# Kernel optimization log

Hardware: AMD Instinct MI355X
Metric: run time of the kernel (lower is better)

## Reference

```python
import jax, jax.numpy as jnp
import numpy as np

N_NODES = 100000
N_EDGES = 1600000
D_IN = 64
D_OUT = 64


def setup_inputs() -> dict:
    key = jax.random.key(0)
    k1, k2, k3, k4, k5, k6, k7 = jax.random.split(key, 7)
    x = jax.random.normal(k1, (N_NODES, D_IN), dtype=jnp.float32)
    edge_index = jax.random.randint(k2, (2, N_EDGES), 0, N_NODES, dtype=jnp.int64)
    pos_encoding = jax.random.normal(k3, (N_NODES, D_IN), dtype=jnp.float32)
    # GCNConv linear weight (no bias inside lin; bias added post-aggregation)
    W_gcn = jax.random.normal(k4, (D_IN, D_OUT), dtype=jnp.float32) / np.sqrt(D_IN)
    b_gcn = jax.random.normal(k5, (D_OUT,), dtype=jnp.float32) * 0.01
    # positional encoding Linear
    W_pos = jax.random.normal(k6, (D_IN, D_OUT), dtype=jnp.float32) / np.sqrt(D_IN)
    b_pos = jax.random.normal(k7, (D_OUT,), dtype=jnp.float32) * 0.01
    return {"x": x, "edge_index": edge_index, "pos_encoding": pos_encoding,
            "W_gcn": W_gcn, "b_gcn": b_gcn, "W_pos": W_pos, "b_pos": b_pos}


def _gcn_conv(x, edge_index, W, b):
    n = x.shape[0]
    # add self-loops (PyG GCNConv default)
    loop = jnp.arange(n, dtype=edge_index.dtype)
    src = jnp.concatenate([edge_index[0], loop])
    dst = jnp.concatenate([edge_index[1], loop])
    # symmetric normalization: deg over destination with unit edge weights
    deg = jax.ops.segment_sum(jnp.ones_like(src, dtype=x.dtype), dst, num_segments=n)
    dinv = jnp.where(deg > 0, jax.lax.rsqrt(deg), 0.0)
    norm = dinv[src] * dinv[dst]  # [E+N]
    h = x @ W  # [N, D_OUT]
    msg = h[src] * norm[:, None]  # gather + scale
    out = jax.ops.segment_sum(msg, dst, num_segments=n)  # scatter-add
    return out + b


def reference(x, edge_index, pos_encoding, W_gcn, b_gcn, W_pos, b_pos):
    conv_out = _gcn_conv(x, edge_index, W_gcn, b_gcn)
    pos = pos_encoding @ W_pos + b_pos
    return conv_out + pos
```

## Files before the change

kernel.cpp:

```cpp
#include <hip/hip_runtime.h>
#include <hip/hip_fp16.h>

#define NN 100000
#define NE 1600000
#define D  64

#define B1    1024
#define BSH   9
#define BMSK  511
#define NB    196
#define M     (NB * B1)

typedef __attribute__((ext_vector_type(8))) _Float16 f16x8;
typedef __attribute__((ext_vector_type(4))) float    f32x4;

__global__ __launch_bounds__(256) void k_hist(const int* __restrict__ dst,
                                              int* __restrict__ hist) {
    __shared__ int h[NB];
    int t = threadIdx.x, blk = blockIdx.x;
    for (int i = t; i < NB; i += 256) h[i] = 0;
    __syncthreads();
    for (int e = blk * 256 + t; e < NE; e += B1 * 256)
        atomicAdd(&h[dst[e] >> BSH], 1);
    __syncthreads();
    for (int i = t; i < NB; i += 256) hist[i * B1 + blk] = h[i];
}

__global__ __launch_bounds__(1024) void k_scanA(int* __restrict__ hist,
                                                int* __restrict__ binsum) {
    __shared__ int ps[1024];
    int t = threadIdx.x, b = blockIdx.x;
    int v = hist[b * B1 + t];
    ps[t] = v;
    __syncthreads();
    for (int off = 1; off < 1024; off <<= 1) {
        int u = (t >= off) ? ps[t - off] : 0;
        __syncthreads();
        ps[t] += u;
        __syncthreads();
    }
    hist[b * B1 + t] = ps[t] - v;
    if (t == 1023) binsum[b] = ps[t];
}

__global__ __launch_bounds__(256) void k_scanB(const int* __restrict__ binsum,
                                               int* __restrict__ binoff) {
    __shared__ int ps[256];
    int t = threadIdx.x;
    int v = (t < NB) ? binsum[t] : 0;
    ps[t] = v;
    __syncthreads();
    for (int off = 1; off < 256; off <<= 1) {
        int u = (t >= off) ? ps[t - off] : 0;
        __syncthreads();
        ps[t] += u;
        __syncthreads();
    }
    if (t < NB) binoff[t] = ps[t] - v;
    if (t == NB - 1) binoff[NB] = ps[t];
}

__global__ __launch_bounds__(256) void k_scatter1(
    const int* __restrict__ src, const int* __restrict__ dst,
    const int* __restrict__ hist, const int* __restrict__ binoff,
    unsigned* __restrict__ ebuf)
{
    __shared__ int cur[NB];
    int t = threadIdx.x, blk = blockIdx.x;
    for (int i = t; i < NB; i += 256)
        cur[i] = binoff[i] + hist[i * B1 + blk];
    __syncthreads();
    for (int e = blk * 256 + t; e < NE; e += B1 * 256) {
        int d = dst[e];
        int p = atomicAdd(&cur[d >> BSH], 1);
        ebuf[p] = ((unsigned)src[e] << BSH) | (unsigned)(d & BMSK);
    }
}

__global__ __launch_bounds__(512) void k_build(
    const int* __restrict__ binoff, const unsigned* __restrict__ ebuf,
    int* __restrict__ rs, float* __restrict__ dinv, int* __restrict__ bucket)
{
    __shared__ int c[512];
    __shared__ int ps[512];
    int t = threadIdx.x, b = blockIdx.x;
    int e0 = binoff[b], e1 = binoff[b + 1];
    c[t] = 0;
    __syncthreads();
    for (int e = e0 + t; e < e1; e += 512)
        atomicAdd(&c[ebuf[e] & BMSK], 1);
    __syncthreads();
    int a = c[t];
    ps[t] = a;
    __syncthreads();
    for (int off = 1; off < 512; off <<= 1) {
        int u = (t >= off) ? ps[t - off] : 0;
        __syncthreads();
        ps[t] += u;
        __syncthreads();
    }
    int p = e0 + ps[t] - a;
    int node = (b << BSH) + t;
    if (node < NN) { rs[node] = p; dinv[node] = rsqrtf((float)(a + 1)); }
    if (b == NB - 1 && t == 0) rs[NN] = NE;
    __syncthreads();
    c[t] = p;
    __syncthreads();
    for (int e = e0 + t; e < e1; e += 512) {
        unsigned u = ebuf[e];
        int pp = atomicAdd(&c[u & BMSK], 1);
        bucket[pp] = (int)(u >> BSH);
    }
}

__global__ __launch_bounds__(256) void k_mm(
    const float* __restrict__ x, const float* __restrict__ Wg,
    const float* __restrict__ dinv, __half* __restrict__ g,
    const float* __restrict__ pos, const float* __restrict__ Wp,
    const float* __restrict__ bg, const float* __restrict__ bp,
    float* __restrict__ out)
{
    __shared__ __align__(16) _Float16 Wt[64][64];
    int t = threadIdx.x;
    int lane = t & 63;
    int wid = t >> 6;
    int half_grid = gridDim.x >> 1;
    bool job2 = blockIdx.x >= half_grid;
    int blk = job2 ? (blockIdx.x - half_grid) : blockIdx.x;
    const float* A = job2 ? pos : x;
    const float* W = job2 ? Wp : Wg;

    for (int i = t; i < 64 * 64; i += 256) {
        int k = i >> 6, n = i & 63;
        Wt[n][k] = (_Float16)W[i];
    }
    __syncthreads();

    int lr = lane & 15;
    int lg = lane >> 4;
    int kofs = lg * 8;

    f16x8 b[4][2];
#pragma unroll
    for (int n = 0; n < 4; ++n)
#pragma unroll
        for (int kt = 0; kt < 2; ++kt)
            b[n][kt] = *(const f16x8*)&Wt[n * 16 + lr][kt * 32 + kofs];

    float bsum[4] = {0.f, 0.f, 0.f, 0.f};
    if (job2) {
#pragma unroll
        for (int n = 0; n < 4; ++n) {
            int c = n * 16 + lr;
            bsum[n] = bg[c] + bp[c];
        }
    }

    for (int rb0 = blk * 64; rb0 < NN; rb0 += half_grid * 64) {
        int rb = rb0 + wid * 16;
        int arow = rb + lr;
        int arc = arow < NN ? arow : NN - 1;
        const float4* ap = (const float4*)(A + (long)arc * 64 + kofs);
        float4 p0 = ap[0], p1 = ap[1], p2 = ap[8], p3 = ap[9];
        f16x8 a0, a1;
        a0[0] = (_Float16)p0.x; a0[1] = (_Float16)p0.y;
        a0[2] = (_Float16)p0.z; a0[3] = (_Float16)p0.w;
        a0[4] = (_Float16)p1.x; a0[5] = (_Float16)p1.y;
        a0[6] = (_Float16)p1.z; a0[7] = (_Float16)p1.w;
        a1[0] = (_Float16)p2.x; a1[1] = (_Float16)p2.y;
        a1[2] = (_Float16)p2.z; a1[3] = (_Float16)p2.w;
        a1[4] = (_Float16)p3.x; a1[5] = (_Float16)p3.y;
        a1[6] = (_Float16)p3.z; a1[7] = (_Float16)p3.w;

        f32x4 z = {0.f, 0.f, 0.f, 0.f};
        f32x4 acc[4] = {z, z, z, z};
#pragma unroll
        for (int n = 0; n < 4; ++n) {
            acc[n] = __builtin_amdgcn_mfma_f32_16x16x32_f16(a0, b[n][0], acc[n], 0, 0, 0);
            acc[n] = __builtin_amdgcn_mfma_f32_16x16x32_f16(a1, b[n][1], acc[n], 0, 0, 0);
        }

        int orow0 = rb + lg * 4;
        if (!job2) {
#pragma unroll
            for (int r = 0; r < 4; ++r) {
                int row = orow0 + r;
                if (row < NN) {
                    float di = dinv[row];
#pragma unroll
                    for (int n = 0; n < 4; ++n)
                        g[(long)row * D + n * 16 + lr] = __float2half(acc[n][r] * di);
                }
            }
        } else {
#pragma unroll
            for (int r = 0; r < 4; ++r) {
                int row = orow0 + r;
                if (row < NN) {
#pragma unroll
                    for (int n = 0; n < 4; ++n)
                        out[(long)row * D + n * 16 + lr] = acc[n][r] + bsum[n];
                }
            }
        }
    }
}

__global__ __launch_bounds__(256) void k_gather(
    const int* __restrict__ rs, const int* __restrict__ bucket,
    const float* __restrict__ dinv, const __half* __restrict__ g,
    float* __restrict__ out)
{
    int lane = threadIdx.x & 63;
    int f = lane & 7;
    int grp = lane >> 3;
    int w0 = (blockIdx.x << 2) + (threadIdx.x >> 6);
    int nw = gridDim.x << 2;
    const uint4* gq = (const uint4*)g;

    for (int n0 = w0; n0 < NN; n0 += nw) {
        int node = __builtin_amdgcn_readfirstlane(n0);
        int r0 = rs[node], r1 = rs[node + 1];
        float a0 = 0.f, a1 = 0.f, a2 = 0.f, a3 = 0.f;
        float a4 = 0.f, a5 = 0.f, a6 = 0.f, a7 = 0.f;
        for (int base = r0; base < r1; base += 64) {
            int nl = r1 - base; if (nl > 64) nl = 64;
            int sl = (lane < nl) ? bucket[base + lane] : 0;
#pragma unroll 2
            for (int c = 0; c < nl; c += 8) {
                int ei = c + grp;
                int s = __shfl(sl, ei);
                if (ei < nl) {
                    uint4 u = gq[(long)s * 8 + f];
                    __half2 h0 = *(__half2*)&u.x, h1 = *(__half2*)&u.y;
                    __half2 h2 = *(__half2*)&u.z, h3 = *(__half2*)&u.w;
                    a0 += __low2float(h0); a1 += __high2float(h0);
                    a2 += __low2float(h1); a3 += __high2float(h1);
                    a4 += __low2float(h2); a5 += __high2float(h2);
                    a6 += __low2float(h3); a7 += __high2float(h3);
                }
            }
        }
#pragma unroll
        for (int mask = 8; mask <= 32; mask <<= 1) {
            a0 += __shfl_xor(a0, mask); a1 += __shfl_xor(a1, mask);
            a2 += __shfl_xor(a2, mask); a3 += __shfl_xor(a3, mask);
            a4 += __shfl_xor(a4, mask); a5 += __shfl_xor(a5, mask);
            a6 += __shfl_xor(a6, mask); a7 += __shfl_xor(a7, mask);
        }
        if (lane < 16) {
            int ff = lane & 7, hs = lane >> 3;
            uint4 u = gq[(long)node * 8 + ff];
            __half2 s0 = hs ? *(__half2*)&u.z : *(__half2*)&u.x;
            __half2 s1 = hs ? *(__half2*)&u.w : *(__half2*)&u.y;
            float b0 = hs ? a4 : a0, b1 = hs ? a5 : a1;
            float b2 = hs ? a6 : a2, b3 = hs ? a7 : a3;
            float di = dinv[node];
            float4* op = (float4*)(out + (long)node * D) + (ff * 2 + hs);
            float4 o = *op;
            o.x += (b0 + __low2float(s0)) * di;
            o.y += (b1 + __high2float(s0)) * di;
            o.z += (b2 + __low2float(s1)) * di;
            o.w += (b3 + __high2float(s1)) * di;
            *op = o;
        }
    }
}

extern "C" void kernel_launch(void* const* d_in, const int* in_sizes, int n_in,
                              void* d_out, int out_size, void* d_ws, size_t ws_size,
                              hipStream_t stream) {
    const float* x   = (const float*)d_in[0];
    const int*   ei  = (const int*)d_in[1];
    const float* pos = (const float*)d_in[2];
    const float* Wg  = (const float*)d_in[3];
    const float* bg  = (const float*)d_in[4];
    const float* Wp  = (const float*)d_in[5];
    const float* bp  = (const float*)d_in[6];
    float* out = (float*)d_out;

    const int* src = ei;
    const int* dst = ei + NE;

    int*      bucket = (int*)d_ws;
    int*      hist   = (int*)d_ws;
    unsigned* ebuf   = (unsigned*)(bucket + NE);
    int*      rs     = (int*)(ebuf + NE);
    float*    dinv   = (float*)(rs + NN + 4);
    __half*   g      = (__half*)(dinv + NN);
    int*      binsum = (int*)(g + (size_t)NN * D);
    int*      binoff = binsum + NB;

    hipLaunchKernelGGL(k_hist,     dim3(B1),   dim3(256),  0, stream, dst, hist);
    hipLaunchKernelGGL(k_scanA,    dim3(NB),   dim3(1024), 0, stream, hist, binsum);
    hipLaunchKernelGGL(k_scanB,    dim3(1),    dim3(256),  0, stream, binsum, binoff);
    hipLaunchKernelGGL(k_scatter1, dim3(B1),   dim3(256),  0, stream, src, dst, hist, binoff, ebuf);
    hipLaunchKernelGGL(k_build,    dim3(NB),   dim3(512),  0, stream, binoff, ebuf, rs, dinv, bucket);
    hipLaunchKernelGGL(k_mm,       dim3(1564), dim3(256),  0, stream,
                       x, Wg, dinv, g, pos, Wp, bg, bp, out);
    hipLaunchKernelGGL(k_gather,   dim3(2048), dim3(256),  0, stream,
                       rs, bucket, dinv, g, out);
}
```

Measured before the change: 215.5 us.

## Fuse histogram and scatter into one pass with per-bin fixed-stride buffers

Replaces the histogram, two-level scan and scatter kernels with one fused kernel. Each block counts its edges per bin in shared memory, reserves a range per bin through global atomics, and writes into fixed-stride per-bin regions. This reads the edge list once instead of twice and removes the large per-block histogram scan. The gather loop drops its per-edge bounds check by padding with a zero row at index NN, and the workspace is aliased so g overlaps ebuf. The fixed bin stride assumes no bin holds more than 16256 edges, which holds for uniform random inputs but could overflow on skewed graphs.

Measured after the change: 217.5 us. No clear change (+0.9%).

```diff
diff --git a/kernel.cpp b/kernel.cpp
--- a/kernel.cpp
+++ b/kernel.cpp
@@ -5,49 +5,56 @@
 #define NE 1600000
 #define D  64
 
-#define B1    1024
-#define BSH   9
-#define BMSK  511
-#define NB    196
-#define M     (NB * B1)
+#define B1     1024
+#define BSH    9
+#define BMSK   511
+#define NB     196
+#define STRIDE 16256
 
 typedef __attribute__((ext_vector_type(8))) _Float16 f16x8;
 typedef __attribute__((ext_vector_type(4))) float    f32x4;
 
-__global__ __launch_bounds__(256) void k_hist(const int* __restrict__ dst,
-                                              int* __restrict__ hist) {
+__global__ __launch_bounds__(256) void k_scatter_fused(
+    const int* __restrict__ src, const int* __restrict__ dst,
+    int* __restrict__ gcnt, unsigned* __restrict__ ebuf)
+{
     __shared__ int h[NB];
     int t = threadIdx.x, blk = blockIdx.x;
     for (int i = t; i < NB; i += 256) h[i] = 0;
     __syncthreads();
-    for (int e = blk * 256 + t; e < NE; e += B1 * 256)
-        atomicAdd(&h[dst[e] >> BSH], 1);
-    __syncthreads();
-    for (int i = t; i < NB; i += 256) hist[i * B1 + blk] = h[i];
-}
-
-__global__ __launch_bounds__(1024) void k_scanA(int* __restrict__ hist,
-                                                int* __restrict__ binsum) {
-    __shared__ int ps[1024];
-    int t = threadIdx.x, b = blockIdx.x;
-    int v = hist[b * B1 + t];
-    ps[t] = v;
-    __syncthreads();
-    for (int off = 1; off < 1024; off <<= 1) {
-        int u = (t >= off) ? ps[t - off] : 0;
-        __syncthreads();
-        ps[t] += u;
-        __syncthreads();
-    }
-    hist[b * B1 + t] = ps[t] - v;
-    if (t == 1023) binsum[b] = ps[t];
-}
-
-__global__ __launch_bounds__(256) void k_scanB(const int* __restrict__ binsum,
-                                               int* __restrict__ binoff) {
+    unsigned v[7]; int bn[7]; int cntl = 0;
+    int e = blk * 256 + t;
+#pragma unroll
+    for (int i = 0; i < 7; ++i, e += B1 * 256) {
+        if (e < NE) {
+            int d = dst[e];
+            int s = src[e];
+            int b = d >> BSH;
+            v[i] = ((unsigned)s << BSH) | (unsigned)(d & BMSK);
+            bn[i] = b;
+            atomicAdd(&h[b], 1);
+            cntl = i + 1;
+        }
+    }
+    __syncthreads();
+    for (int i = t; i < NB; i += 256)
+        h[i] = atomicAdd(&gcnt[i], h[i]);
+    __syncthreads();
+#pragma unroll
+    for (int i = 0; i < 7; ++i) {
+        if (i < cntl) {
+            int b = bn[i];
+            int p = atomicAdd(&h[b], 1);
+            ebuf[b * STRIDE + p] = v[i];
+        }
+    }
+}
+
+__global__ __launch_bounds__(256) void k_scan196(const int* __restrict__ gcnt,
+                                                 int* __restrict__ binoff) {
     __shared__ int ps[256];
     int t = threadIdx.x;
-    int v = (t < NB) ? binsum[t] : 0;
+    int v = (t < NB) ? gcnt[t] : 0;
     ps[t] = v;
     __syncthreads();
     for (int off = 1; off < 256; off <<= 1) {
@@ -60,35 +67,21 @@
     if (t == NB - 1) binoff[NB] = ps[t];
 }
 
-__global__ __launch_bounds__(256) void k_scatter1(
-    const int* __restrict__ src, const int* __restrict__ dst,
-    const int* __restrict__ hist, const int* __restrict__ binoff,
-    unsigned* __restrict__ ebuf)
-{
-    __shared__ int cur[NB];
-    int t = threadIdx.x, blk = blockIdx.x;
-    for (int i = t; i < NB; i += 256)
-        cur[i] = binoff[i] + hist[i * B1 + blk];
-    __syncthreads();
-    for (int e = blk * 256 + t; e < NE; e += B1 * 256) {
-        int d = dst[e];
-        int p = atomicAdd(&cur[d >> BSH], 1);
-        ebuf[p] = ((unsigned)src[e] << BSH) | (unsigned)(d & BMSK);
-    }
-}
-
 __global__ __launch_bounds__(512) void k_build(
-    const int* __restrict__ binoff, const unsigned* __restrict__ ebuf,
+    const int* __restrict__ gcnt, const int* __restrict__ binoff,
+    const unsigned* __restrict__ ebuf,
     int* __restrict__ rs, float* __restrict__ dinv, int* __restrict__ bucket)
 {
     __shared__ int c[512];
     __shared__ int ps[512];
     int t = threadIdx.x, b = blockIdx.x;
-    int e0 = binoff[b], e1 = binoff[b + 1];
+    int e0s = b * STRIDE;
+    int cnt = gcnt[b];
+    int g0  = binoff[b];
     c[t] = 0;
     __syncthreads();
-    for (int e = e0 + t; e < e1; e += 512)
-        atomicAdd(&c[ebuf[e] & BMSK], 1);
+    for (int e = t; e < cnt; e += 512)
+        atomicAdd(&c[ebuf[e0s + e] & BMSK], 1);
     __syncthreads();
     int a = c[t];
     ps[t] = a;
@@ -99,15 +92,15 @@
         ps[t] += u;
         __syncthreads();
     }
-    int p = e0 + ps[t] - a;
+    int p = g0 + ps[t] - a;
     int node = (b << BSH) + t;
     if (node < NN) { rs[node] = p; dinv[node] = rsqrtf((float)(a + 1)); }
     if (b == NB - 1 && t == 0) rs[NN] = NE;
     __syncthreads();
     c[t] = p;
     __syncthreads();
-    for (int e = e0 + t; e < e1; e += 512) {
-        unsigned u = ebuf[e];
+    for (int e = t; e < cnt; e += 512) {
+        unsigned u = ebuf[e0s + e];
         int pp = atomicAdd(&c[u & BMSK], 1);
         bucket[pp] = (int)(u >> BSH);
     }
@@ -130,6 +123,8 @@
     const float* A = job2 ? pos : x;
     const float* W = job2 ? Wp : Wg;
 
+    if (blockIdx.x == 0 && t < 64) g[(long)NN * D + t] = __float2half(0.f);
+
     for (int i = t; i < 64 * 64; i += 256) {
         int k = i >> 6, n = i & 63;
         Wt[n][k] = (_Float16)W[i];
@@ -151,8 +146,8 @@
     if (job2) {
 #pragma unroll
         for (int n = 0; n < 4; ++n) {
-            int c = n * 16 + lr;
-            bsum[n] = bg[c] + bp[c];
+            int cc = n * 16 + lr;
+            bsum[n] = bg[cc] + bp[cc];
         }
     }
 
@@ -224,21 +219,20 @@
         float a0 = 0.f, a1 = 0.f, a2 = 0.f, a3 = 0.f;
         float a4 = 0.f, a5 = 0.f, a6 = 0.f, a7 = 0.f;
         for (int base = r0; base < r1; base += 64) {
-            int nl = r1 - base; if (nl > 64) nl = 64;
-            int sl = (lane < nl) ? bucket[base + lane] : 0;
-#pragma unroll 2
-            for (int c = 0; c < nl; c += 8) {
-                int ei = c + grp;
-                int s = __shfl(sl, ei);
-                if (ei < nl) {
-                    uint4 u = gq[(long)s * 8 + f];
-                    __half2 h0 = *(__half2*)&u.x, h1 = *(__half2*)&u.y;
-                    __half2 h2 = *(__half2*)&u.z, h3 = *(__half2*)&u.w;
-                    a0 += __low2float(h0); a1 += __high2float(h0);
-                    a2 += __low2float(h1); a3 += __high2float(h1);
-                    a4 += __low2float(h2); a5 += __high2float(h2);
-                    a6 += __low2float(h3); a7 += __high2float(h3);
-                }
+            int rem = r1 - base;
+            int nl = rem < 64 ? rem : 64;
+            int sl = (lane < nl) ? bucket[base + lane] : NN;
+            int NG = (nl + 7) >> 3;
+#pragma unroll 4
+            for (int c = 0; c < NG; ++c) {
+                int s = __shfl(sl, c * 8 + grp);
+                uint4 u = gq[(long)s * 8 + f];
+                __half2 h0 = *(__half2*)&u.x, h1 = *(__half2*)&u.y;
+                __half2 h2 = *(__half2*)&u.z, h3 = *(__half2*)&u.w;
+                a0 += __low2float(h0); a1 += __high2float(h0);
+                a2 += __low2float(h1); a3 += __high2float(h1);
+                a4 += __low2float(h2); a5 += __high2float(h2);
+                a6 += __low2float(h3); a7 += __high2float(h3);
             }
         }
 #pragma unroll
@@ -282,22 +276,23 @@
     const int* src = ei;
     const int* dst = ei + NE;
 
-    int*      bucket = (int*)d_ws;
-    int*      hist   = (int*)d_ws;
-    unsigned* ebuf   = (unsigned*)(bucket + NE);
-    int*      rs     = (int*)(ebuf + NE);
+    char* Wb = (char*)d_ws;
+    __half*   g      = (__half*)Wb;
+    unsigned* ebuf   = (unsigned*)Wb;
+    int*      bucket = (int*)(Wb + 12800256);
+    int*      rs     = bucket + NE;
     float*    dinv   = (float*)(rs + NN + 4);
-    __half*   g      = (__half*)(dinv + NN);
-    int*      binsum = (int*)(g + (size_t)NN * D);
-    int*      binoff = binsum + NB;
-
-    hipLaunchKernelGGL(k_hist,     dim3(B1),   dim3(256),  0, stream, dst, hist);
-    hipLaunchKernelGGL(k_scanA,    dim3(NB),   dim3(1024), 0, stream, hist, binsum);
-    hipLaunchKernelGGL(k_scanB,    dim3(1),    dim3(256),  0, stream, binsum, binoff);
-    hipLaunchKernelGGL(k_scatter1, dim3(B1),   dim3(256),  0, stream, src, dst, hist, binoff, ebuf);
-    hipLaunchKernelGGL(k_build,    dim3(NB),   dim3(512),  0, stream, binoff, ebuf, rs, dinv, bucket);
-    hipLaunchKernelGGL(k_mm,       dim3(1564), dim3(256),  0, stream,
+    int*      gcnt   = (int*)(dinv + NN);
+    int*      binoff = gcnt + NB;
+
+    hipMemsetAsync(gcnt, 0, NB * sizeof(int), stream);
+    hipLaunchKernelGGL(k_scatter_fused, dim3(B1),   dim3(256), 0, stream,
+                       src, dst, gcnt, ebuf);
+    hipLaunchKernelGGL(k_scan196,       dim3(1),    dim3(256), 0, stream, gcnt, binoff);
+    hipLaunchKernelGGL(k_build,         dim3(NB),   dim3(512), 0, stream,
+                       gcnt, binoff, ebuf, rs, dinv, bucket);
+    hipLaunchKernelGGL(k_mm,            dim3(1564), dim3(256), 0, stream,
                        x, Wg, dinv, g, pos, Wp, bg, bp, out);
-    hipLaunchKernelGGL(k_gather,   dim3(2048), dim3(256),  0, stream,
+    hipLaunchKernelGGL(k_gather,        dim3(2048), dim3(256), 0, stream,
                        rs, bucket, dinv, g, out);
 }
```

## Replace CSR build and pull gather with bin-local LDS atomic scatter aggregation

Applied to the files above, without the earlier changes.

Drops the per-node CSR construction (second counting sort into bucket and rs). Edges are left coarsely binned by 256-node destination ranges, and each bin is aggregated by one 1024-thread block that accumulates into LDS with float atomics before a final per-node write. The aim is to remove the k_build pass and the per-node irregular loops. In exchange the gather becomes LDS-atomic-bound, runs with only 391 blocks, and sums in a nondeterministic order.

Result: slower. 853.0 us (+295.9%).

```diff
diff --git a/kernel.cpp b/kernel.cpp
--- a/kernel.cpp
+++ b/kernel.cpp
@@ -5,11 +5,10 @@
 #define NE 1600000
 #define D  64
 
-#define B1    1024
-#define BSH   9
-#define BMSK  511
-#define NB    196
-#define M     (NB * B1)
+#define B1   1024
+#define BSH  8
+#define BMSK 255
+#define NB   391
 
 typedef __attribute__((ext_vector_type(8))) _Float16 f16x8;
 typedef __attribute__((ext_vector_type(4))) float    f32x4;
@@ -27,7 +26,7 @@
 }
 
 __global__ __launch_bounds__(1024) void k_scanA(int* __restrict__ hist,
-                                                int* __restrict__ binsum) {
+                                                int* __restrict__ bsum) {
     __shared__ int ps[1024];
     int t = threadIdx.x, b = blockIdx.x;
     int v = hist[b * B1 + t];
@@ -40,17 +39,17 @@
         __syncthreads();
     }
     hist[b * B1 + t] = ps[t] - v;
-    if (t == 1023) binsum[b] = ps[t];
-}
-
-__global__ __launch_bounds__(256) void k_scanB(const int* __restrict__ binsum,
+    if (t == 1023) bsum[b] = ps[t];
+}
+
+__global__ __launch_bounds__(512) void k_scanB(const int* __restrict__ bsum,
                                                int* __restrict__ binoff) {
-    __shared__ int ps[256];
+    __shared__ int ps[512];
     int t = threadIdx.x;
-    int v = (t < NB) ? binsum[t] : 0;
+    int v = (t < NB) ? bsum[t] : 0;
     ps[t] = v;
     __syncthreads();
-    for (int off = 1; off < 256; off <<= 1) {
+    for (int off = 1; off < 512; off <<= 1) {
         int u = (t >= off) ? ps[t - off] : 0;
         __syncthreads();
         ps[t] += u;
@@ -77,39 +76,20 @@
     }
 }
 
-__global__ __launch_bounds__(512) void k_build(
-    const int* __restrict__ binoff, const unsigned* __restrict__ ebuf,
-    int* __restrict__ rs, float* __restrict__ dinv, int* __restrict__ bucket)
-{
-    __shared__ int c[512];
-    __shared__ int ps[512];
+__global__ __launch_bounds__(1024) void k_count(const int* __restrict__ binoff,
+                                                const unsigned* __restrict__ ebuf,
+                                                float* __restrict__ dinv) {
+    __shared__ int c[256];
     int t = threadIdx.x, b = blockIdx.x;
+    if (t < 256) c[t] = 0;
+    __syncthreads();
     int e0 = binoff[b], e1 = binoff[b + 1];
-    c[t] = 0;
-    __syncthreads();
-    for (int e = e0 + t; e < e1; e += 512)
+    for (int e = e0 + t; e < e1; e += 1024)
         atomicAdd(&c[ebuf[e] & BMSK], 1);
     __syncthreads();
-    int a = c[t];
-    ps[t] = a;
-    __syncthreads();
-    for (int off = 1; off < 512; off <<= 1) {
-        int u = (t >= off) ? ps[t - off] : 0;
-        __syncthreads();
-        ps[t] += u;
-        __syncthreads();
-    }
-    int p = e0 + ps[t] - a;
-    int node = (b << BSH) + t;
-    if (node < NN) { rs[node] = p; dinv[node] = rsqrtf((float)(a + 1)); }
-    if (b == NB - 1 && t == 0) rs[NN] = NE;
-    __syncthreads();
-    c[t] = p;
-    __syncthreads();
-    for (int e = e0 + t; e < e1; e += 512) {
-        unsigned u = ebuf[e];
-        int pp = atomicAdd(&c[u & BMSK], 1);
-        bucket[pp] = (int)(u >> BSH);
+    if (t < 256) {
+        int node = (b << BSH) + t;
+        if (node < NN) dinv[node] = rsqrtf((float)(c[t] + 1));
     }
 }
 
@@ -151,8 +131,8 @@
     if (job2) {
 #pragma unroll
         for (int n = 0; n < 4; ++n) {
-            int c = n * 16 + lr;
-            bsum[n] = bg[c] + bp[c];
+            int cc = n * 16 + lr;
+            bsum[n] = bg[cc] + bp[cc];
         }
     }
 
@@ -206,63 +186,51 @@
     }
 }
 
-__global__ __launch_bounds__(256) void k_gather(
-    const int* __restrict__ rs, const int* __restrict__ bucket,
+__global__ __launch_bounds__(1024) void k_gather(
+    const int* __restrict__ binoff, const unsigned* __restrict__ ebuf,
     const float* __restrict__ dinv, const __half* __restrict__ g,
     float* __restrict__ out)
 {
-    int lane = threadIdx.x & 63;
-    int f = lane & 7;
-    int grp = lane >> 3;
-    int w0 = (blockIdx.x << 2) + (threadIdx.x >> 6);
-    int nw = gridDim.x << 2;
-    const uint4* gq = (const uint4*)g;
-
-    for (int n0 = w0; n0 < NN; n0 += nw) {
-        int node = __builtin_amdgcn_readfirstlane(n0);
-        int r0 = rs[node], r1 = rs[node + 1];
-        float a0 = 0.f, a1 = 0.f, a2 = 0.f, a3 = 0.f;
-        float a4 = 0.f, a5 = 0.f, a6 = 0.f, a7 = 0.f;
-        for (int base = r0; base < r1; base += 64) {
-            int nl = r1 - base; if (nl > 64) nl = 64;
-            int sl = (lane < nl) ? bucket[base + lane] : 0;
-#pragma unroll 2
-            for (int c = 0; c < nl; c += 8) {
-                int ei = c + grp;
-                int s = __shfl(sl, ei);
-                if (ei < nl) {
-                    uint4 u = gq[(long)s * 8 + f];
-                    __half2 h0 = *(__half2*)&u.x, h1 = *(__half2*)&u.y;
-                    __half2 h2 = *(__half2*)&u.z, h3 = *(__half2*)&u.w;
-                    a0 += __low2float(h0); a1 += __high2float(h0);
-                    a2 += __low2float(h1); a3 += __high2float(h1);
-                    a4 += __low2float(h2); a5 += __high2float(h2);
-                    a6 += __low2float(h3); a7 += __high2float(h3);
-                }
+    __shared__ float accE[256 * 32];
+    __shared__ float accO[256 * 32];
+    int t = threadIdx.x, b = blockIdx.x;
+    for (int i = t; i < 256 * 32; i += 1024) { accE[i] = 0.f; accO[i] = 0.f; }
+    __syncthreads();
+
+    int e0 = binoff[b], e1 = binoff[b + 1];
+    int lane = t & 63;
+    int hl = lane >> 5;
+    int l  = lane & 31;
+    int w  = t >> 6;
+    const unsigned* gw = (const unsigned*)g;
+
+    for (int base = e0 + w * 8; base < e1; base += 16 * 8) {
+#pragma unroll
+        for (int k = 0; k < 4; ++k) {
+            int e = base + k * 2 + hl;
+            if (e < e1) {
+                unsigned u = ebuf[e];
+                int s  = (int)(u >> BSH);
+                int dl = (int)(u & BMSK);
+                unsigned gd = gw[(long)s * 32 + l];
+                __half2 hh = *(__half2*)&gd;
+                atomicAdd(&accE[dl * 32 + l], __low2float(hh));
+                atomicAdd(&accO[dl * 32 + l], __high2float(hh));
             }
         }
-#pragma unroll
-        for (int mask = 8; mask <= 32; mask <<= 1) {
-            a0 += __shfl_xor(a0, mask); a1 += __shfl_xor(a1, mask);
-            a2 += __shfl_xor(a2, mask); a3 += __shfl_xor(a3, mask);
-            a4 += __shfl_xor(a4, mask); a5 += __shfl_xor(a5, mask);
-            a6 += __shfl_xor(a6, mask); a7 += __shfl_xor(a7, mask);
-        }
-        if (lane < 16) {
-            int ff = lane & 7, hs = lane >> 3;
-            uint4 u = gq[(long)node * 8 + ff];
-            __half2 s0 = hs ? *(__half2*)&u.z : *(__half2*)&u.x;
-            __half2 s1 = hs ? *(__half2*)&u.w : *(__half2*)&u.y;
-            float b0 = hs ? a4 : a0, b1 = hs ? a5 : a1;
-            float b2 = hs ? a6 : a2, b3 = hs ? a7 : a3;
+    }
+    __syncthreads();
+
+    int r = t >> 6;
+    for (int p = 0; p < 16; ++p) {
+        int row = p * 16 + r;
+        int node = (b << BSH) + row;
+        if (node < NN) {
             float di = dinv[node];
-            float4* op = (float4*)(out + (long)node * D) + (ff * 2 + hs);
-            float4 o = *op;
-            o.x += (b0 + __low2float(s0)) * di;
-            o.y += (b1 + __high2float(s0)) * di;
-            o.z += (b2 + __low2float(s1)) * di;
-            o.w += (b3 + __high2float(s1)) * di;
-            *op = o;
+            float gs = __half2float(g[(long)node * 64 + lane]);
+            float av = (lane & 1) ? accO[row * 32 + (lane >> 1)]
+                                  : accE[row * 32 + (lane >> 1)];
+            out[(long)node * 64 + lane] += (av + gs) * di;
         }
     }
 }
@@ -282,22 +250,22 @@
     const int* src = ei;
     const int* dst = ei + NE;
 
-    int*      bucket = (int*)d_ws;
-    int*      hist   = (int*)d_ws;
-    unsigned* ebuf   = (unsigned*)(bucket + NE);
-    int*      rs     = (int*)(ebuf + NE);
-    float*    dinv   = (float*)(rs + NN + 4);
-    __half*   g      = (__half*)(dinv + NN);
-    int*      binsum = (int*)(g + (size_t)NN * D);
-    int*      binoff = binsum + NB;
+    unsigned* ebuf   = (unsigned*)d_ws;
+    __half*   g      = (__half*)(ebuf + NE);
+    int*      hist   = (int*)(g + (size_t)NN * D);
+    int*      bsum   = hist + NB * B1;
+    int*      binoff = bsum + 512;
+    float*    dinv   = (float*)(binoff + 512);
 
     hipLaunchKernelGGL(k_hist,     dim3(B1),   dim3(256),  0, stream, dst, hist);
-    hipLaunchKernelGGL(k_scanA,    dim3(NB),   dim3(1024), 0, stream, hist, binsum);
-    hipLaunchKernelGGL(k_scanB,    dim3(1),    dim3(256),  0, stream, binsum, binoff);
-    hipLaunchKernelGGL(k_scatter1, dim3(B1),   dim3(256),  0, stream, src, dst, hist, binoff, ebuf);
-    hipLaunchKernelGGL(k_build,    dim3(NB),   dim3(512),  0, stream, binoff, ebuf, rs, dinv, bucket);
+    hipLaunchKernelGGL(k_scanA,    dim3(NB),   dim3(1024), 0, stream, hist, bsum);
+    hipLaunchKernelGGL(k_scanB,    dim3(1),    dim3(512),  0, stream, bsum, binoff);
+    hipLaunchKernelGGL(k_scatter1, dim3(B1),   dim3(256),  0, stream,
+                       src, dst, hist, binoff, ebuf);
+    hipLaunchKernelGGL(k_count,    dim3(NB),   dim3(1024), 0, stream,
+                       binoff, ebuf, dinv);
     hipLaunchKernelGGL(k_mm,       dim3(1564), dim3(256),  0, stream,
                        x, Wg, dinv, g, pos, Wp, bg, bp, out);
-    hipLaunchKernelGGL(k_gather,   dim3(2048), dim3(256),  0, stream,
-                       rs, bucket, dinv, g, out);
-}
+    hipLaunchKernelGGL(k_gather,   dim3(NB),   dim3(1024), 0, stream,
+                       binoff, ebuf, dinv, g, out);
+}
```

## Halve bin size, cache bin edges in LDS, pad gather with zero row

Applied to the files above, without the earlier changes.

The coarse bucketing bins shrink from 512 to 256 nodes, giving 391 bins. The build kernel now stages each bin's packed edges in shared memory so the second pass reads LDS instead of re-reading global memory, with a fallback to global memory when a bin overflows the cache. The gather loop drops its per-edge bounds check by pointing padding lanes at a zeroed sentinel row NN of g, written by k_mm, and unrolls the loop 4 times. The workspace layout is rearranged to fit the sentinel row and the larger scan buffers, at the cost of more scan blocks and more shared memory per build block.

New measurement: 218.3 us. About the same (+1.3%).

```diff
diff --git a/kernel.cpp b/kernel.cpp
--- a/kernel.cpp
+++ b/kernel.cpp
@@ -5,11 +5,11 @@
 #define NE 1600000
 #define D  64
 
-#define B1    1024
-#define BSH   9
-#define BMSK  511
-#define NB    196
-#define M     (NB * B1)
+#define B1   1024
+#define BSH  8
+#define BMSK 255
+#define NB   391
+#define CAP  4864
 
 typedef __attribute__((ext_vector_type(8))) _Float16 f16x8;
 typedef __attribute__((ext_vector_type(4))) float    f32x4;
@@ -27,7 +27,7 @@
 }
 
 __global__ __launch_bounds__(1024) void k_scanA(int* __restrict__ hist,
-                                                int* __restrict__ binsum) {
+                                                int* __restrict__ bsum) {
     __shared__ int ps[1024];
     int t = threadIdx.x, b = blockIdx.x;
     int v = hist[b * B1 + t];
@@ -40,17 +40,17 @@
         __syncthreads();
     }
     hist[b * B1 + t] = ps[t] - v;
-    if (t == 1023) binsum[b] = ps[t];
-}
-
-__global__ __launch_bounds__(256) void k_scanB(const int* __restrict__ binsum,
+    if (t == 1023) bsum[b] = ps[t];
+}
+
+__global__ __launch_bounds__(512) void k_scanB(const int* __restrict__ bsum,
                                                int* __restrict__ binoff) {
-    __shared__ int ps[256];
+    __shared__ int ps[512];
     int t = threadIdx.x;
-    int v = (t < NB) ? binsum[t] : 0;
+    int v = (t < NB) ? bsum[t] : 0;
     ps[t] = v;
     __syncthreads();
-    for (int off = 1; off < 256; off <<= 1) {
+    for (int off = 1; off < 512; off <<= 1) {
         int u = (t >= off) ? ps[t - off] : 0;
         __syncthreads();
         ps[t] += u;
@@ -81,33 +81,39 @@
     const int* __restrict__ binoff, const unsigned* __restrict__ ebuf,
     int* __restrict__ rs, float* __restrict__ dinv, int* __restrict__ bucket)
 {
-    __shared__ int c[512];
-    __shared__ int ps[512];
+    __shared__ unsigned cache[CAP];
+    __shared__ int c[256];
+    __shared__ int ps[256];
     int t = threadIdx.x, b = blockIdx.x;
     int e0 = binoff[b], e1 = binoff[b + 1];
-    c[t] = 0;
-    __syncthreads();
-    for (int e = e0 + t; e < e1; e += 512)
-        atomicAdd(&c[ebuf[e] & BMSK], 1);
-    __syncthreads();
-    int a = c[t];
-    ps[t] = a;
-    __syncthreads();
-    for (int off = 1; off < 512; off <<= 1) {
-        int u = (t >= off) ? ps[t - off] : 0;
-        __syncthreads();
-        ps[t] += u;
-        __syncthreads();
-    }
-    int p = e0 + ps[t] - a;
-    int node = (b << BSH) + t;
-    if (node < NN) { rs[node] = p; dinv[node] = rsqrtf((float)(a + 1)); }
+    int cnt = e1 - e0;
+    if (t < 256) c[t] = 0;
+    __syncthreads();
+    for (int i = t; i < cnt; i += 512) {
+        unsigned u = ebuf[e0 + i];
+        if (i < CAP) cache[i] = u;
+        atomicAdd(&c[u & BMSK], 1);
+    }
+    __syncthreads();
+    int a = (t < 256) ? c[t] : 0;
+    if (t < 256) ps[t] = a;
+    __syncthreads();
+    for (int off = 1; off < 256; off <<= 1) {
+        int u2 = (t >= off && t < 256) ? ps[t - off] : 0;
+        __syncthreads();
+        if (t < 256) ps[t] += u2;
+        __syncthreads();
+    }
+    if (t < 256) {
+        int p = e0 + ps[t] - a;
+        int node = (b << BSH) + t;
+        if (node < NN) { rs[node] = p; dinv[node] = rsqrtf((float)(a + 1)); }
+        c[t] = p;
+    }
     if (b == NB - 1 && t == 0) rs[NN] = NE;
     __syncthreads();
-    c[t] = p;
-    __syncthreads();
-    for (int e = e0 + t; e < e1; e += 512) {
-        unsigned u = ebuf[e];
+    for (int i = t; i < cnt; i += 512) {
+        unsigned u = (i < CAP) ? cache[i] : ebuf[e0 + i];
         int pp = atomicAdd(&c[u & BMSK], 1);
         bucket[pp] = (int)(u >> BSH);
     }
@@ -130,6 +136,8 @@
     const float* A = job2 ? pos : x;
     const float* W = job2 ? Wp : Wg;
 
+    if (blockIdx.x == 0 && t < 64) g[(long)NN * D + t] = __float2half(0.f);
+
     for (int i = t; i < 64 * 64; i += 256) {
         int k = i >> 6, n = i & 63;
         Wt[n][k] = (_Float16)W[i];
@@ -151,8 +159,8 @@
     if (job2) {
 #pragma unroll
         for (int n = 0; n < 4; ++n) {
-            int c = n * 16 + lr;
-            bsum[n] = bg[c] + bp[c];
+            int cc = n * 16 + lr;
+            bsum[n] = bg[cc] + bp[cc];
         }
     }
 
@@ -224,21 +232,20 @@
         float a0 = 0.f, a1 = 0.f, a2 = 0.f, a3 = 0.f;
         float a4 = 0.f, a5 = 0.f, a6 = 0.f, a7 = 0.f;
         for (int base = r0; base < r1; base += 64) {
-            int nl = r1 - base; if (nl > 64) nl = 64;
-            int sl = (lane < nl) ? bucket[base + lane] : 0;
-#pragma unroll 2
-            for (int c = 0; c < nl; c += 8) {
-                int ei = c + grp;
-                int s = __shfl(sl, ei);
-                if (ei < nl) {
-                    uint4 u = gq[(long)s * 8 + f];
-                    __half2 h0 = *(__half2*)&u.x, h1 = *(__half2*)&u.y;
-                    __half2 h2 = *(__half2*)&u.z, h3 = *(__half2*)&u.w;
-                    a0 += __low2float(h0); a1 += __high2float(h0);
-                    a2 += __low2float(h1); a3 += __high2float(h1);
-                    a4 += __low2float(h2); a5 += __high2float(h2);
-                    a6 += __low2float(h3); a7 += __high2float(h3);
-                }
+            int rem = r1 - base;
+            int nl = rem < 64 ? rem : 64;
+            int sl = (lane < nl) ? bucket[base + lane] : NN;
+            int NG = (nl + 7) >> 3;
+#pragma unroll 4
+            for (int c = 0; c < NG; ++c) {
+                int s = __shfl(sl, c * 8 + grp);
+                uint4 u = gq[(long)s * 8 + f];
+                __half2 h0 = *(__half2*)&u.x, h1 = *(__half2*)&u.y;
+                __half2 h2 = *(__half2*)&u.z, h3 = *(__half2*)&u.w;
+                a0 += __low2float(h0); a1 += __high2float(h0);
+                a2 += __low2float(h1); a3 += __high2float(h1);
+                a4 += __low2float(h2); a5 += __high2float(h2);
+                a6 += __low2float(h3); a7 += __high2float(h3);
             }
         }
 #pragma unroll
@@ -282,20 +289,23 @@
     const int* src = ei;
     const int* dst = ei + NE;
 
-    int*      bucket = (int*)d_ws;
-    int*      hist   = (int*)d_ws;
-    unsigned* ebuf   = (unsigned*)(bucket + NE);
-    int*      rs     = (int*)(ebuf + NE);
+    char* Wb = (char*)d_ws;
+    unsigned* ebuf   = (unsigned*)Wb;
+    __half*   g      = (__half*)(Wb + 6400000);
+    int*      bucket = (int*)(Wb + 19200128);
+    int*      hist   = bucket;
+    int*      rs     = (int*)(Wb + 25600128);
     float*    dinv   = (float*)(rs + NN + 4);
-    __half*   g      = (__half*)(dinv + NN);
-    int*      binsum = (int*)(g + (size_t)NN * D);
-    int*      binoff = binsum + NB;
+    int*      bsum   = (int*)(dinv + NN);
+    int*      binoff = bsum + 512;
 
     hipLaunchKernelGGL(k_hist,     dim3(B1),   dim3(256),  0, stream, dst, hist);
-    hipLaunchKernelGGL(k_scanA,    dim3(NB),   dim3(1024), 0, stream, hist, binsum);
-    hipLaunchKernelGGL(k_scanB,    dim3(1),    dim3(256),  0, stream, binsum, binoff);
-    hipLaunchKernelGGL(k_scatter1, dim3(B1),   dim3(256),  0, stream, src, dst, hist, binoff, ebuf);
-    hipLaunchKernelGGL(k_build,    dim3(NB),   dim3(512),  0, stream, binoff, ebuf, rs, dinv, bucket);
+    hipLaunchKernelGGL(k_scanA,    dim3(NB),   dim3(1024), 0, stream, hist, bsum);
+    hipLaunchKernelGGL(k_scanB,    dim3(1),    dim3(512),  0, stream, bsum, binoff);
+    hipLaunchKernelGGL(k_scatter1, dim3(B1),   dim3(256),  0, stream,
+                       src, dst, hist, binoff, ebuf);
+    hipLaunchKernelGGL(k_build,    dim3(NB),   dim3(512),  0, stream,
+                       binoff, ebuf, rs, dinv, bucket);
     hipLaunchKernelGGL(k_mm,       dim3(1564), dim3(256),  0, stream,
                        x, Wg, dinv, g, pos, Wp, bg, bp, out);
     hipLaunchKernelGGL(k_gather,   dim3(2048), dim3(256),  0, stream,
```
